# Performance work log

Measured on AMD Instinct MI355X. Metric: run time of the kernel, lower is better.

Reference implementation:

```python
import jax, jax.numpy as jnp
import numpy as np

EPS = 1e-12  # F.normalize default eps

def _l2norm(v):
    # torch F.normalize: v / max(||v||, eps)
    n = jnp.sqrt(jnp.sum(v * v, axis=-1, keepdims=True))
    return v / jnp.maximum(n, EPS)

def setup_inputs() -> dict:
    key = jax.random.key(0)
    k1, k2, k3 = jax.random.split(key, 3)
    bn, cn, d = 8192, 16384, 512
    x = jax.random.normal(k1, (bn, d), dtype=jnp.float32)
    positive = jax.random.normal(k2, (bn, d), dtype=jnp.float32)
    negative = jax.random.normal(k3, (cn, d), dtype=jnp.float32)
    return {"x": x, "positive": positive, "negative": negative}

def reference(x, positive, negative):
    # normalize x and positive explicitly (as in the torch code);
    # cosine_similarity(x_n, negative) == x_n @ normalize(negative).T since x_n is unit-norm
    xn = _l2norm(x)            # (bn, d)
    pn = _l2norm(positive)     # (bn, d)
    nn_ = _l2norm(negative)    # (cn, d)
    sim = jnp.sum(xn * pn, axis=1)                 # (bn,) positive cosine sim
    logits = jnp.einsum('bd,cd->bc', xn, nn_)      # (bn, cn) cosine sims vs negatives
    denom = jnp.sum(jnp.exp(logits), axis=1)       # (bn,) -- logits bounded in [-1,1], safe
    bn = x.shape[0]
    loss = -jnp.sum(sim - jnp.log(denom)) / bn
    return loss
```

## Files before the change

### kernel.cpp

```cpp
#include <hip/hip_runtime.h>
#include <stdint.h>

#define D 512
#define BNROWS 8192
#define CNROWS 16384
#define NPART 256

typedef __attribute__((ext_vector_type(4))) float f32x4;
typedef __attribute__((ext_vector_type(8))) __bf16 bf16x8;
typedef __attribute__((ext_vector_type(8))) short s16x8;

typedef const __attribute__((address_space(1))) unsigned int* gas_ptr;
typedef __attribute__((address_space(3))) unsigned int* las_ptr;

__device__ __forceinline__ void gload_lds16(const void* g, void* l) {
    __builtin_amdgcn_global_load_lds((gas_ptr)g, (las_ptr)l, 16, 0, 0);
}

__device__ __forceinline__ short f2bf(float f) {
    uint32_t u = __float_as_uint(f);
    uint32_t r = (u + 0x7FFFu + ((u >> 16) & 1u)) >> 16;
    return (short)r;
}

__device__ __forceinline__ float wave_reduce_add(float v) {
#pragma unroll
    for (int m = 32; m >= 1; m >>= 1) v += __shfl_xor(v, m, 64);
    return v;
}

__global__ __launch_bounds__(256) void k_norm(const float* __restrict__ x,
                                              const float* __restrict__ p,
                                              const float* __restrict__ n,
                                              short* __restrict__ xnb,
                                              short* __restrict__ nnb,
                                              float* __restrict__ sim) {
    const int wid = threadIdx.x >> 6, lane = threadIdx.x & 63;
    if (blockIdx.x < BNROWS / 4) {
        const int row = blockIdx.x * 4 + wid;
        const float* xr = x + (size_t)row * D + lane * 8;
        const float* pr = p + (size_t)row * D + lane * 8;
        f32x4 x0 = *(const f32x4*)xr, x1 = *(const f32x4*)(xr + 4);
        f32x4 p0 = *(const f32x4*)pr, p1 = *(const f32x4*)(pr + 4);
        float xx = 0.f, pp = 0.f, xp = 0.f;
#pragma unroll
        for (int j = 0; j < 4; ++j) {
            xx += x0[j] * x0[j] + x1[j] * x1[j];
            pp += p0[j] * p0[j] + p1[j] * p1[j];
            xp += x0[j] * p0[j] + x1[j] * p1[j];
        }
        xx = wave_reduce_add(xx);
        pp = wave_reduce_add(pp);
        xp = wave_reduce_add(xp);
        const float rx = 1.0f / fmaxf(sqrtf(xx), 1e-12f);
        const float rp = 1.0f / fmaxf(sqrtf(pp), 1e-12f);
        if (lane == 0) sim[row] = xp * rx * rp;
        s16x8 o;
#pragma unroll
        for (int j = 0; j < 4; ++j) {
            o[j] = f2bf(x0[j] * rx);
            o[j + 4] = f2bf(x1[j] * rx);
        }
        *(s16x8*)(xnb + (size_t)row * D + lane * 8) = o;
    } else {
        const int row = (blockIdx.x - BNROWS / 4) * 4 + wid;
        const float* nr = n + (size_t)row * D + lane * 8;
        f32x4 n0 = *(const f32x4*)nr, n1 = *(const f32x4*)(nr + 4);
        float nn = 0.f;
#pragma unroll
        for (int j = 0; j < 4; ++j) nn += n0[j] * n0[j] + n1[j] * n1[j];
        nn = wave_reduce_add(nn);
        const float rn = 1.0f / fmaxf(sqrtf(nn), 1e-12f);
        s16x8 o;
#pragma unroll
        for (int j = 0; j < 4; ++j) {
            o[j] = f2bf(n0[j] * rn);
            o[j + 4] = f2bf(n1[j] * rn);
        }
        *(s16x8*)(nnb + (size_t)row * D + lane * 8) = o;
    }
}


#define LOAD_A(buf, mh)                                                                  \
    {                                                                                    \
        _Pragma("unroll") for (int m2 = 0; m2 < 4; ++m2) _Pragma("unroll") for (int ks = \
                                                                                    0;   \
                                                                                ks < 2;  \
                                                                                ++ks)    \
            af[m2 * 2 + ks] =                                                            \
            *(const bf16x8*)(Ard[buf] + (mh)*512 + m2 * 128 + ks * 4096);                \
    }
#define LOAD_B(buf, nh)                                                                  \
    {                                                                                    \
        _Pragma("unroll") for (int n2 = 0; n2 < 2; ++n2) _Pragma("unroll") for (int ks = \
                                                                                    0;   \
                                                                                ks < 2;  \
                                                                                ++ks)    \
            bfr[((nh)*2 + n2) * 2 + ks] =                                                \
            *(const bf16x8*)(Brd[buf] + ((nh)*2 + n2) * 128 + ks * 4096);                \
    }
#define MMA(mh, nh)                                                                     \
    {                                                                                   \
        _Pragma("unroll") for (int m2 = 0; m2 < 4; ++m2)                                \
            _Pragma("unroll") for (int n2 = 0; n2 < 2; ++n2)                            \
                _Pragma("unroll") for (int ks = 0; ks < 2; ++ks) acc[(mh)*4 + m2]       \
                                                                   [(nh)*2 + n2] =     \
                __builtin_amdgcn_mfma_f32_16x16x32_bf16(af[m2 * 2 + ks],                \
                                                        bfr[((nh)*2 + n2) * 2 + ks],   \
                                                        acc[(mh)*4 + m2][(nh)*2 + n2], \
                                                        0, 0, 0);                      \
    }
#define STAGE_A(buf, h, kt)                                      \
    {                                                            \
        gload_lds16(agp[h] + (kt)*64, dstA[buf][h]);             \
        gload_lds16(agp[h] + (kt)*64 + 32, dstA[buf][h] + 4096); \
    }
#define STAGE_B(buf, h, kt)                                      \
    {                                                            \
        gload_lds16(bgp[h] + (kt)*64, dstB[buf][h]);             \
        gload_lds16(bgp[h] + (kt)*64 + 32, dstB[buf][h] + 4096); \
    }
#define BAR() __builtin_amdgcn_s_barrier()
#define LGKM0() asm volatile("s_waitcnt lgkmcnt(0)" ::: "memory")
#define PRIO1() __builtin_amdgcn_s_setprio(1)
#define PRIO0() __builtin_amdgcn_s_setprio(0)
#define VMC4() asm volatile("s_waitcnt vmcnt(4)" ::: "memory")
#define VMC0() asm volatile("s_waitcnt vmcnt(0)" ::: "memory")

#define ITER(t0, ST)                                                          \
    {                                                                         \
               \
        LOAD_A(0, 0); LOAD_B(0, 0); LOAD_B(0, 1);                             \
        STAGE_A(1, 0, (t0) + 1); STAGE_A(1, 1, (t0) + 1);                     \
        BAR(); LGKM0(); PRIO1(); MMA(0, 0); MMA(0, 1); PRIO0(); BAR();        \
                               \
        LOAD_A(0, 1);                                                         \
        if (ST) { STAGE_B(0, 0, (t0) + 2); STAGE_B(0, 1, (t0) + 2); }         \
        BAR(); LGKM0(); PRIO1(); MMA(1, 0); MMA(1, 1); PRIO0();               \
        if (ST) VMC4(); else VMC0();                                          \
        BAR();                                                                \
                             \
        LOAD_A(1, 0); LOAD_B(1, 0); LOAD_B(1, 1);                             \
        if (ST) { STAGE_A(0, 0, (t0) + 2); STAGE_A(0, 1, (t0) + 2); }         \
        BAR(); LGKM0(); PRIO1(); MMA(0, 0); MMA(0, 1); PRIO0(); BAR();        \
                             \
        LOAD_A(1, 1);                                                         \
        if (ST) { STAGE_B(1, 0, (t0) + 3); STAGE_B(1, 1, (t0) + 3); }         \
        BAR(); LGKM0(); PRIO1(); MMA(1, 0); MMA(1, 1); PRIO0();               \
        if (ST) VMC4();                                                       \
        BAR();                                                                \
    }

__global__ __launch_bounds__(512, 2) void k_gemm_exp(const short* __restrict__ A,
                                                     const short* __restrict__ B,
                                                     float* __restrict__ part) {
    __shared__ short lds[2][2][2][8][128][8];

    const int t = threadIdx.x;
    const int lane = t & 63, wid = t >> 6;
    const int wr = wid >> 2, wc = wid & 3;
    const int lg = lane >> 4, lm = lane & 15;

    const uint32_t g = blockIdx.x + gridDim.x * blockIdx.y;
    const int xcd = g & 7;
    const int r_ = g >> 3;
    const int bx = (xcd << 3) | (r_ & 7);
    const int by = r_ >> 3;
    const int blockM = by * 256;
    const int blockN = bx * 256;

    const int row_s = t & 127, kg_s = t >> 7;
    const short* agp[2];
    const short* bgp[2];
    short* dstA[2][2];
    short* dstB[2][2];
#pragma unroll
    for (int h = 0; h < 2; ++h) {
        agp[h] = A + (size_t)(blockM + h * 128 + row_s) * D + kg_s * 8;
        bgp[h] = B + (size_t)(blockN + h * 128 + row_s) * D + kg_s * 8;
#pragma unroll
        for (int buf = 0; buf < 2; ++buf) {
            dstA[buf][h] = &lds[buf][0][h][kg_s][row_s][0];
            dstB[buf][h] = &lds[buf][1][h][kg_s][row_s][0];
        }
    }
    const short* Ard[2];
    const short* Brd[2];
#pragma unroll
    for (int buf = 0; buf < 2; ++buf) {
        Ard[buf] = &lds[buf][0][wr][lg][lm][0];
        Brd[buf] = &lds[buf][1][wc >> 1][lg][(wc & 1) * 64 + lm][0];
    }

    f32x4 acc[8][4];
#pragma unroll
    for (int i = 0; i < 8; ++i)
#pragma unroll
        for (int j = 0; j < 4; ++j) acc[i][j] = (f32x4){0.f, 0.f, 0.f, 0.f};

    bf16x8 af[8], bfr[8];

    STAGE_A(0, 0, 0);
    STAGE_A(0, 1, 0);
    STAGE_B(0, 0, 0);
    STAGE_B(0, 1, 0);
    STAGE_B(1, 0, 1);
    STAGE_B(1, 1, 1);
    VMC4();
    BAR();

    for (int i = 0; i < 3; ++i) {
        const int t0 = 2 * i;
        ITER(t0, 1);
    }
    ITER(6, 0);

    const int pcol = bx * 4 + wc;
    float* prow = part + (size_t)(blockM + wr * 128) * NPART + pcol;
#pragma unroll
    for (int mi = 0; mi < 8; ++mi) {
#pragma unroll
        for (int r = 0; r < 4; ++r) {
            float s = 0.f;
#pragma unroll
            for (int ni = 0; ni < 4; ++ni) s += __expf(acc[mi][ni][r]);
            s += __shfl_xor(s, 1, 64);
            s += __shfl_xor(s, 2, 64);
            s += __shfl_xor(s, 4, 64);
            s += __shfl_xor(s, 8, 64);
            if (lm == 0) prow[(size_t)(mi * 16 + lg * 4 + r) * NPART] = s;
        }
    }
}

__global__ __launch_bounds__(256) void k_final1(const float* __restrict__ part,
                                                const float* __restrict__ sim,
                                                float* __restrict__ bterm) {
    __shared__ float red[4];
    const int wid = threadIdx.x >> 6, lane = threadIdx.x & 63;
    const int row = blockIdx.x * 4 + wid;
    f32x4 v = *(const f32x4*)(part + (size_t)row * NPART + lane * 4);
    float s = v[0] + v[1] + v[2] + v[3];
    s = wave_reduce_add(s);
    float term = 0.f;
    if (lane == 0) term = sim[row] - logf(s);
    if (lane == 0) red[wid] = term;
    __syncthreads();
    if (threadIdx.x == 0)
        bterm[blockIdx.x] = red[0] + red[1] + red[2] + red[3];
}

__global__ __launch_bounds__(256) void k_final2(const float* __restrict__ bterm,
                                                float* __restrict__ out) {
    __shared__ float red[4];
    float s = 0.f;
    for (int i = threadIdx.x; i < BNROWS / 4; i += 256) s += bterm[i];
    s = wave_reduce_add(s);
    const int wid = threadIdx.x >> 6, lane = threadIdx.x & 63;
    if (lane == 0) red[wid] = s;
    __syncthreads();
    if (threadIdx.x == 0) {
        float tot = red[0] + red[1] + red[2] + red[3];
        out[0] = -tot / (float)BNROWS;
    }
}

extern "C" void kernel_launch(void* const* d_in, const int* in_sizes, int n_in,
                              void* d_out, int out_size, void* d_ws, size_t ws_size,
                              hipStream_t stream) {
    const float* x = (const float*)d_in[0];
    const float* p = (const float*)d_in[1];
    const float* n = (const float*)d_in[2];
    char* ws = (char*)d_ws;
    short* xnb = (short*)ws;
    short* nnb = (short*)(ws + (size_t)8 * 1024 * 1024);
    float* sim = (float*)(ws + (size_t)24 * 1024 * 1024);
    float* part = (float*)(ws + (size_t)24 * 1024 * 1024 + 64 * 1024);
    float* bterm = (float*)(ws + (size_t)33 * 1024 * 1024);
    float* out = (float*)d_out;

    k_norm<<<dim3(BNROWS / 4 + CNROWS / 4), dim3(256), 0, stream>>>(x, p, n, xnb, nnb,
                                                                    sim);
    k_gemm_exp<<<dim3(CNROWS / 256, BNROWS / 256), dim3(512), 0, stream>>>(xnb, nnb,
                                                                           part);
    k_final1<<<dim3(BNROWS / 4), dim3(256), 0, stream>>>(part, sim, bterm);
    k_final2<<<dim3(1), dim3(256), 0, stream>>>(bterm, out);
}
```

Measured before the change: 286.9 us.

## Make GEMM blocks persistent over eight N-tiles with a continuous cross-tile pipeline

The GEMM-exp kernel now launches 256 blocks instead of a 64x32 grid. Each block keeps one 256-row M tile and walks 8 consecutive 256-column N tiles in one unbroken K loop. Staging addresses are computed from a global step index, so loads for the next N tile are already in flight while the exp/reduce epilogue for the finished tile runs. This removes per-tile prologue and drain bubbles and the launch tail. The cost is that only 256 blocks exist for a kernel whose launch bounds allow two per CU, so there is less inter-block latency hiding and a single block per CU may leave the device underoccupied. The old XCD-aware block swizzle is replaced by a simpler mapping.

Measured after the change: 1.059 ms. 269% more time.

```diff
diff --git a/kernel.cpp b/kernel.cpp
--- a/kernel.cpp
+++ b/kernel.cpp
@@ -111,15 +111,18 @@
                                                         acc[(mh)*4 + m2][(nh)*2 + n2], \
                                                         0, 0, 0);                      \
     }
-#define STAGE_A(buf, h, kt)                                      \
-    {                                                            \
-        gload_lds16(agp[h] + (kt)*64, dstA[buf][h]);             \
-        gload_lds16(agp[h] + (kt)*64 + 32, dstA[buf][h] + 4096); \
-    }
-#define STAGE_B(buf, h, kt)                                      \
-    {                                                            \
-        gload_lds16(bgp[h] + (kt)*64, dstB[buf][h]);             \
-        gload_lds16(bgp[h] + (kt)*64 + 32, dstB[buf][h] + 4096); \
+#define STAGE_A(buf, h, s)                                                    \
+    {                                                                         \
+        const short* ga = agp[h] + (size_t)((s)&7) * 64;                      \
+        gload_lds16(ga, dstA[buf][h]);                                        \
+        gload_lds16(ga + 32, dstA[buf][h] + 4096);                            \
+    }
+#define STAGE_B(buf, h, s)                                                    \
+    {                                                                         \
+        const short* gb = bgp[h] + (size_t)((s) >> 3) * (256 * (size_t)D) +   \
+                          (size_t)((s)&7) * 64;                               \
+        gload_lds16(gb, dstB[buf][h]);                                        \
+        gload_lds16(gb + 32, dstB[buf][h] + 4096);                            \
     }
 #define BAR() __builtin_amdgcn_s_barrier()
 #define LGKM0() asm volatile("s_waitcnt lgkmcnt(0)" ::: "memory")
@@ -130,22 +133,18 @@
 
 #define ITER(t0, ST)                                                          \
     {                                                                         \
-               \
-        LOAD_A(0, 0); LOAD_B(0, 0); LOAD_B(0, 1);                             \
+         LOAD_A(0, 0); LOAD_B(0, 0); LOAD_B(0, 1);                     \
         STAGE_A(1, 0, (t0) + 1); STAGE_A(1, 1, (t0) + 1);                     \
         BAR(); LGKM0(); PRIO1(); MMA(0, 0); MMA(0, 1); PRIO0(); BAR();        \
-                               \
-        LOAD_A(0, 1);                                                         \
+         LOAD_A(0, 1);                                                 \
         if (ST) { STAGE_B(0, 0, (t0) + 2); STAGE_B(0, 1, (t0) + 2); }         \
         BAR(); LGKM0(); PRIO1(); MMA(1, 0); MMA(1, 1); PRIO0();               \
         if (ST) VMC4(); else VMC0();                                          \
         BAR();                                                                \
-                             \
-        LOAD_A(1, 0); LOAD_B(1, 0); LOAD_B(1, 1);                             \
+         LOAD_A(1, 0); LOAD_B(1, 0); LOAD_B(1, 1);                     \
         if (ST) { STAGE_A(0, 0, (t0) + 2); STAGE_A(0, 1, (t0) + 2); }         \
         BAR(); LGKM0(); PRIO1(); MMA(0, 0); MMA(0, 1); PRIO0(); BAR();        \
-                             \
-        LOAD_A(1, 1);                                                         \
+         LOAD_A(1, 1);                                                 \
         if (ST) { STAGE_B(1, 0, (t0) + 3); STAGE_B(1, 1, (t0) + 3); }         \
         BAR(); LGKM0(); PRIO1(); MMA(1, 0); MMA(1, 1); PRIO0();               \
         if (ST) VMC4();                                                       \
@@ -162,13 +161,10 @@
     const int wr = wid >> 2, wc = wid & 3;
     const int lg = lane >> 4, lm = lane & 15;
 
-    const uint32_t g = blockIdx.x + gridDim.x * blockIdx.y;
-    const int xcd = g & 7;
-    const int r_ = g >> 3;
-    const int bx = (xcd << 3) | (r_ & 7);
-    const int by = r_ >> 3;
+    const int by = blockIdx.x & 31;
+    const int g = blockIdx.x >> 5;
     const int blockM = by * 256;
-    const int blockN = bx * 256;
+    const int bxBase = g * 8;
 
     const int row_s = t & 127, kg_s = t >> 7;
     const short* agp[2];
@@ -178,7 +174,7 @@
 #pragma unroll
     for (int h = 0; h < 2; ++h) {
         agp[h] = A + (size_t)(blockM + h * 128 + row_s) * D + kg_s * 8;
-        bgp[h] = B + (size_t)(blockN + h * 128 + row_s) * D + kg_s * 8;
+        bgp[h] = B + (size_t)(bxBase * 256 + h * 128 + row_s) * D + kg_s * 8;
 #pragma unroll
         for (int buf = 0; buf < 2; ++buf) {
             dstA[buf][h] = &lds[buf][0][h][kg_s][row_s][0];
@@ -210,26 +206,35 @@
     VMC4();
     BAR();
 
-    for (int i = 0; i < 3; ++i) {
-        const int t0 = 2 * i;
-        ITER(t0, 1);
-    }
-    ITER(6, 0);
-
-    const int pcol = bx * 4 + wc;
-    float* prow = part + (size_t)(blockM + wr * 128) * NPART + pcol;
-#pragma unroll
-    for (int mi = 0; mi < 8; ++mi) {
-#pragma unroll
-        for (int r = 0; r < 4; ++r) {
-            float s = 0.f;
-#pragma unroll
-            for (int ni = 0; ni < 4; ++ni) s += __expf(acc[mi][ni][r]);
-            s += __shfl_xor(s, 1, 64);
-            s += __shfl_xor(s, 2, 64);
-            s += __shfl_xor(s, 4, 64);
-            s += __shfl_xor(s, 8, 64);
-            if (lm == 0) prow[(size_t)(mi * 16 + lg * 4 + r) * NPART] = s;
+    for (int it = 0; it < 32; ++it) {
+        const int t0 = 2 * it;
+        if (it < 31) {
+            ITER(t0, 1);
+        } else {
+            ITER(t0, 0);
+        }
+        if ((it & 3) == 3) {
+            const int j = it >> 2;
+            const int pcol = (bxBase + j) * 4 + wc;
+            float* prow = part + (size_t)(blockM + wr * 128) * NPART + pcol;
+#pragma unroll
+            for (int mi = 0; mi < 8; ++mi) {
+#pragma unroll
+                for (int r = 0; r < 4; ++r) {
+                    float s = 0.f;
+#pragma unroll
+                    for (int ni = 0; ni < 4; ++ni) s += __expf(acc[mi][ni][r]);
+                    s += __shfl_xor(s, 1, 64);
+                    s += __shfl_xor(s, 2, 64);
+                    s += __shfl_xor(s, 4, 64);
+                    s += __shfl_xor(s, 8, 64);
+                    if (lm == 0) prow[(size_t)(mi * 16 + lg * 4 + r) * NPART] = s;
+                }
+            }
+#pragma unroll
+            for (int i = 0; i < 8; ++i)
+#pragma unroll
+                for (int q = 0; q < 4; ++q) acc[i][q] = (f32x4){0.f, 0.f, 0.f, 0.f};
         }
     }
 }
@@ -282,8 +287,7 @@
 
     k_norm<<<dim3(BNROWS / 4 + CNROWS / 4), dim3(256), 0, stream>>>(x, p, n, xnb, nnb,
                                                                     sim);
-    k_gemm_exp<<<dim3(CNROWS / 256, BNROWS / 256), dim3(512), 0, stream>>>(xnb, nnb,
-                                                                           part);
+    k_gemm_exp<<<dim3(256), dim3(512), 0, stream>>>(xnb, nnb, part);
     k_final1<<<dim3(BNROWS / 4), dim3(256), 0, stream>>>(part, sim, bterm);
     k_final2<<<dim3(1), dim3(256), 0, stream>>>(bterm, out);
 }
```
